# Optimization experiments

Measured on AMD Instinct MI355X. Metric: run time of the kernel, lower is better.

## Reference

```python
import jax, jax.numpy as jnp
import numpy as np

# PercentClosenessBoosting (not in provided source): standard form is
#   new_boost = boost_tensor + (1 - tensor / tensor.max()) * boost_percent
# i.e. units far from the max get boosted more.

def _fwd_math(x, boost_tensor, sparsity, boost_percent):
    B, E = x.shape
    # --- run_boosting ---
    new_boost = boost_tensor + (1.0 - x / jnp.max(x)) * boost_percent
    boosted = jnp.maximum(x, 0.0) + new_boost
    # inhibition tensor starts empty -> apply_sparse_self_affector is a no-op
    # --- run_k_winners_positive: top-k (max_active) per row of boosted, binarize ---
    order = jnp.argsort(-boosted, axis=1)          # descending sort indices
    rank = jnp.argsort(order, axis=1)              # rank of each element in its row
    max_active = jnp.ceil(sparsity[1] * E)
    saved = jnp.where((rank < max_active) & (boosted > 0), 1.0, 0.0)  # ctx.save_for_backward
    # --- choose_boosted_to_satisfy_minimum (note: GLOBAL sum vs per-row min, faithful) ---
    min_active = jnp.floor(sparsity[0] * E)
    active = jnp.sum(saved)
    to_activate = jnp.ceil(min_active - active)
    border = jnp.argsort(-new_boost, axis=1)
    brank = jnp.argsort(border, axis=1)
    need = active < min_active
    out = jnp.where(need & (brank < to_activate), 1.0, saved)
    # --- zero boost where active ---
    final_boost = jnp.where(out > 0, jnp.zeros_like(new_boost), new_boost)
    return out, final_boost, saved


def setup_inputs() -> dict:
    key = jax.random.key(0)
    k1, = jax.random.split(key, 1)
    B, E = 64, 131072
    x = jax.random.normal(k1, (B, E), dtype=jnp.float32)
    boost_tensor = jnp.zeros((B, E), dtype=jnp.float32)
    sparsity = jnp.array([0.002, 0.02], dtype=jnp.float32)
    boost_percent = jnp.float32(1e-8)
    return {"x": x, "boost_tensor": boost_tensor, "sparsity": sparsity, "boost_percent": boost_percent}


def reference(x, boost_tensor, sparsity, boost_percent):
    out, final_boost, _ = _fwd_math(x, boost_tensor, sparsity, boost_percent)
    return out, final_boost
```

## Files before the change

kernel.cpp:

```cpp
#include <hip/hip_runtime.h>

#define BR 64
#define EC 131072
#define CAP 8192
#define LCAP 1024
#define CHUNKS 16
#define CHUNK_V (EC / CHUNKS / 4)
#define NSCH 41
#define NS (NSCH * 64)
#define SSTRIDE 3197
#define BINS 4096

typedef float nf4 __attribute__((ext_vector_type(4)));

#define WS_GMAX 0
#define WS_ACTIVE 1
#define WS_TOACT 2
#define WS_UT 136
#define WS_CUT 200
#define WS_CCNT 264
#define WS_UT2 512
#define WS_CUT2 576
#define WS_BMAX 1024
#define CAND_U_OFF 4096
#define CAND_I_OFF (CAND_U_OFF + BR * CAP)

__device__ __forceinline__ unsigned map_f(float f) {
    unsigned b = __float_as_uint(f);
    return (b & 0x80000000u) ? ~b : (b | 0x80000000u);
}
__device__ __forceinline__ float unmap_f(unsigned u) {
    unsigned b = (u & 0x80000000u) ? (u & 0x7FFFFFFFu) : ~u;
    return __uint_as_float(b);
}

__device__ __forceinline__ void compute_vals(float x, float bt, float gmax, float bp,
                                             float* nb, float* bo) {
#pragma clang fp contract(off)
    float q = x / gmax;
    float t = 1.0f - q;
    float p = t * bp;
    float nbv = bt + p;
    *nb = nbv;
    *bo = fmaxf(x, 0.0f) + nbv;
}

__device__ __forceinline__ unsigned umax_(unsigned a, unsigned b) { return a > b ? a : b; }

__device__ __forceinline__ unsigned calc_K(const float* sp) {
    unsigned K = (unsigned)ceilf(sp[1] * (float)EC);
    if (K > EC) K = EC;
    if (K == 0) K = 1;
    return K;
}

__device__ unsigned lds_radix_select(const unsigned* su, unsigned n, unsigned K,
                                     unsigned* hist, unsigned* scan, unsigned* sb,
                                     int t, unsigned* krem) {
    unsigned pv = 0, Kp = K;
    for (int pass = 0; pass < 4; ++pass) {
        int shift = 24 - 8 * pass;
        hist[t] = 0;
        __syncthreads();
        for (unsigned i = t; i < n; i += 256) {
            unsigned u = su[i];
            bool match = (pass == 0) || ((u >> (shift + 8)) == (pv >> (shift + 8)));
            if (match) atomicAdd(&hist[(u >> shift) & 0xFFu], 1u);
        }
        __syncthreads();
        unsigned my = hist[t];
        scan[t] = my;
        __syncthreads();
        for (int off = 1; off < 256; off <<= 1) {
            unsigned v = (t + off < 256) ? scan[t + off] : 0u;
            __syncthreads();
            scan[t] += v;
            __syncthreads();
        }
        unsigned incl = scan[t], excl = incl - my;
        if (excl < Kp && incl >= Kp) {
            sb[0] = pv | ((unsigned)t << shift);
            sb[1] = Kp - excl;
        }
        __syncthreads();
        pv = sb[0];
        Kp = sb[1];
        __syncthreads();
    }
    *krem = Kp;
    return pv;
}

template<int USE_NB>
__device__ unsigned row_select_full(const float* xr, const float* br, float gmax,
                                    float bp, unsigned K, unsigned* hist,
                                    unsigned* aux, int t,
                                    unsigned* ut_out, unsigned* cut_out) {
    unsigned prefix = 0, Kp = K;
    for (int pass = 0; pass < 4; ++pass) {
        int shift = 24 - 8 * pass;
        hist[t] = 0;
        __syncthreads();
        for (int i = t; i < EC; i += 256) {
            float nb, bo;
            compute_vals(xr[i], br[i], gmax, bp, &nb, &bo);
            unsigned u = map_f(USE_NB ? nb : bo);
            bool match = (pass == 0) || ((u >> (shift + 8)) == (prefix >> (shift + 8)));
            if (match) atomicAdd(&hist[(u >> shift) & 0xFFu], 1u);
        }
        __syncthreads();
        if (t == 0) {
            unsigned cum = 0, bsel = 0, kr = Kp;
            for (int b = 255; b >= 0; --b) {
                unsigned h = hist[b];
                if (cum + h >= Kp) { bsel = (unsigned)b; kr = Kp - cum; break; }
                cum += h;
            }
            aux[0] = prefix | (bsel << shift);
            aux[1] = kr;
        }
        __syncthreads();
        prefix = aux[0];
        Kp = aux[1];
        __syncthreads();
    }
    unsigned u_t = prefix, ties = Kp;
    if (t == 0) { aux[6] = 0; aux[7] = 0xFFFFFFFFu; }
    __syncthreads();
    int wid = t >> 6, lane = t & 63;
    for (int base0 = 0; base0 < EC; base0 += 256) {
        int i = base0 + t;
        float nb, bo;
        compute_vals(xr[i], br[i], gmax, bp, &nb, &bo);
        bool eq = (map_f(USE_NB ? nb : bo) == u_t);
        unsigned long long bal = __ballot(eq);
        if (lane == 0) aux[2 + wid] = (unsigned)__popcll(bal);
        __syncthreads();
        unsigned run = aux[6];
        unsigned wpre = 0;
        for (int w = 0; w < wid; ++w) wpre += aux[2 + w];
        if (eq) {
            unsigned r = run + wpre + (unsigned)__popcll(bal & ((1ull << lane) - 1ull));
            if (r == ties - 1) aux[7] = (unsigned)i;
        }
        __syncthreads();
        if (t == 0) aux[6] = run + aux[2] + aux[3] + aux[4] + aux[5];
        __syncthreads();
        if (aux[6] >= ties) break;
    }
    if (t == 0) { *ut_out = u_t; *cut_out = aux[7]; }
    __syncthreads();
    return u_t;
}

__global__ __launch_bounds__(256) void kA(const float4* __restrict__ x4,
                                          unsigned* __restrict__ ws) {
    if (blockIdx.x == 0)
        for (int i = threadIdx.x; i < 1024; i += 256) ws[i] = 0u;
    unsigned m = 0;
    const int nvec = BR * EC / 4;
    int stride = gridDim.x * 256;
    for (int v = blockIdx.x * 256 + threadIdx.x; v < nvec; v += stride) {
        float4 xv = x4[v];
        m = umax_(m, map_f(xv.x)); m = umax_(m, map_f(xv.y));
        m = umax_(m, map_f(xv.z)); m = umax_(m, map_f(xv.w));
    }
    for (int off = 32; off; off >>= 1) m = umax_(m, __shfl_down(m, off, 64));
    __shared__ unsigned sm[4];
    if ((threadIdx.x & 63) == 0) sm[threadIdx.x >> 6] = m;
    __syncthreads();
    if (threadIdx.x == 0)
        ws[WS_BMAX + blockIdx.x] = umax_(umax_(sm[0], sm[1]), umax_(sm[2], sm[3]));
}

__global__ __launch_bounds__(256) void kB(const float* __restrict__ x,
                                          const float* __restrict__ bt,
                                          const float* __restrict__ sp,
                                          const float* __restrict__ bp_p,
                                          unsigned* __restrict__ ws) {
    __shared__ unsigned hist[BINS];
    __shared__ unsigned lu[LCAP], li[LCAP];
    __shared__ unsigned ssum[256], sabove[256];
    __shared__ unsigned sred[4];
    __shared__ unsigned stlo, slcnt, sgbase;
    int t = threadIdx.x;
    int row = blockIdx.x >> 4, chunk = blockIdx.x & (CHUNKS - 1);

    unsigned m = 0;
    for (int i = t; i < 1024; i += 256) m = umax_(m, ws[WS_BMAX + i]);
    for (int off = 32; off; off >>= 1) m = umax_(m, __shfl_down(m, off, 64));
    if ((t & 63) == 0) sred[t >> 6] = m;
    __syncthreads();
    unsigned gmu = umax_(umax_(sred[0], sred[1]), umax_(sred[2], sred[3]));
    if (blockIdx.x == 0 && t == 0) ws[WS_GMAX] = gmu;
    float gmax = unmap_f(gmu);
    float bp = *bp_p;

    for (int i = t; i < BINS; i += 256) hist[i] = 0;
    if (t == 0) slcnt = 0;
    __syncthreads();
    const float* xr = x + (size_t)row * EC;
    const float* br = bt + (size_t)row * EC;
    for (int s = t; s < NS; s += 256) {
        int idx = (s >> 6) * SSTRIDE + (s & 63);
        float nb, bo;
        compute_vals(xr[idx], br[idx], gmax, bp, &nb, &bo);
        atomicAdd(&hist[map_f(bo) >> 20], 1u);
    }
    __syncthreads();

    unsigned K = calc_K(sp);
    unsigned R = (unsigned)ceilf(1.75f * (float)NS * (float)K / (float)EC);
    if (R < 32) R = 32;
    if (R > NS) R = NS;
    unsigned hv[16];
    unsigned s = 0;
    #pragma unroll
    for (int j = 0; j < 16; ++j) { hv[j] = hist[t * 16 + j]; s += hv[j]; }
    ssum[t] = s;
    __syncthreads();
    if (t == 0) {
        unsigned acc = 0;
        for (int q = 255; q >= 0; --q) { sabove[q] = acc; acc += ssum[q]; }
    }
    __syncthreads();
    unsigned cum = sabove[t];
    for (int j = 15; j >= 0; --j) {
        unsigned h = hv[j];
        if (cum < R && cum + h >= R) stlo = ((unsigned)(t * 16 + j)) << 20;
        cum += h;
    }
    __syncthreads();
    unsigned tlo = stlo ? stlo - 1u : 0u;

    const float4* x4 = (const float4*)x;
    const float4* bt4 = (const float4*)bt;
    unsigned* cu = ws + CAND_U_OFF + (size_t)row * CAP;
    unsigned* ci = ws + CAND_I_OFF + (size_t)row * CAP;
    size_t base = (size_t)row * (EC / 4) + (size_t)chunk * CHUNK_V;
    int ebase = chunk * (EC / CHUNKS);
    for (int v = t; v < CHUNK_V; v += 256) {
        float4 xv = x4[base + v];
        float4 bv = bt4[base + v];
        float xs[4] = {xv.x, xv.y, xv.z, xv.w};
        float bs[4] = {bv.x, bv.y, bv.z, bv.w};
        #pragma unroll
        for (int j = 0; j < 4; ++j) {
            float nb, bo;
            compute_vals(xs[j], bs[j], gmax, bp, &nb, &bo);
            unsigned u = map_f(bo);
            if (u > tlo) {
                unsigned p = atomicAdd(&slcnt, 1u);
                if (p < LCAP) {
                    lu[p] = u; li[p] = (unsigned)(ebase + v * 4 + j);
                } else {
                    unsigned gp = atomicAdd(&ws[WS_CCNT + row], 1u);
                    if (gp < CAP) { cu[gp] = u; ci[gp] = (unsigned)(ebase + v * 4 + j); }
                }
            }
        }
    }
    __syncthreads();
    unsigned n = slcnt < LCAP ? slcnt : LCAP;
    if (t == 0) sgbase = atomicAdd(&ws[WS_CCNT + row], n);
    __syncthreads();
    unsigned gb = sgbase;
    for (unsigned i = t; i < n; i += 256) {
        unsigned gp = gb + i;
        if (gp < CAP) { cu[gp] = lu[i]; ci[gp] = li[i]; }
    }
}

__global__ __launch_bounds__(256) void kC(const float* __restrict__ x,
                                          const float* __restrict__ bt,
                                          const float* __restrict__ sp,
                                          const float* __restrict__ bp_p,
                                          unsigned* __restrict__ ws) {
    int row = blockIdx.x;
    int t = threadIdx.x;
    unsigned n = ws[WS_CCNT + row];
    unsigned K = calc_K(sp);
    __shared__ unsigned su[CAP];
    __shared__ unsigned hist[256], scan[256], sb[2];
    __shared__ unsigned marr[256];
    __shared__ unsigned mcnt;
    __shared__ unsigned aux[8];
    __shared__ unsigned scnt[4];
    unsigned row_active = 0;
    if (n >= K && n <= CAP) {
        const unsigned* cu = ws + CAND_U_OFF + (size_t)row * CAP;
        const unsigned* ci = ws + CAND_I_OFF + (size_t)row * CAP;
        for (unsigned i = t; i < n; i += 256) su[i] = cu[i];
        if (t == 0) mcnt = 0;
        __syncthreads();
        unsigned krem2;
        unsigned u_t = lds_radix_select(su, n, K, hist, scan, sb, t, &krem2);
        for (unsigned i = t; i < n; i += 256)
            if (su[i] == u_t) {
                unsigned p = atomicAdd(&mcnt, 1u);
                if (p < 256) marr[p] = ci[i];
            }
        __syncthreads();
        unsigned m = mcnt;
        if (m <= 256) {
            for (unsigned i = t; i < m; i += 256) {
                unsigned myidx = marr[i];
                unsigned r = 0;
                for (unsigned j = 0; j < m; ++j) r += (marr[j] < myidx) ? 1u : 0u;
                if (r == krem2 - 1) { ws[WS_UT + row] = u_t; ws[WS_CUT + row] = myidx; }
            }
        } else {
            for (unsigned i = t; i < n; i += 256) {
                if (su[i] == u_t) {
                    unsigned myidx = ci[i];
                    unsigned r = 0;
                    for (unsigned j = 0; j < n; ++j)
                        if (su[j] == u_t && ci[j] < myidx) ++r;
                    if (r == krem2 - 1) { ws[WS_UT + row] = u_t; ws[WS_CUT + row] = myidx; }
                }
            }
        }
        if (u_t > 0x80000000u) {
            row_active = K;
        } else {
            unsigned c = 0;
            for (unsigned i = t; i < n; i += 256) c += (su[i] > 0x80000000u) ? 1u : 0u;
            for (int off = 32; off; off >>= 1) c += __shfl_down(c, off, 64);
            if ((t & 63) == 0) scnt[t >> 6] = c;
            __syncthreads();
            row_active = scnt[0] + scnt[1] + scnt[2] + scnt[3];
        }
    } else {
        float gmax = unmap_f(ws[WS_GMAX]);
        float bp = *bp_p;
        const float* xr = x + (size_t)row * EC;
        const float* br = bt + (size_t)row * EC;
        unsigned u_t = row_select_full<0>(xr, br, gmax, bp, K, hist, aux, t,
                                          &ws[WS_UT + row], &ws[WS_CUT + row]);
        if (u_t > 0x80000000u) {
            row_active = K;
        } else {
            unsigned c = 0;
            for (int i = t; i < EC; i += 256) {
                float nb, bo;
                compute_vals(xr[i], br[i], gmax, bp, &nb, &bo);
                c += (map_f(bo) > 0x80000000u) ? 1u : 0u;
            }
            for (int off = 32; off; off >>= 1) c += __shfl_down(c, off, 64);
            if ((t & 63) == 0) scnt[t >> 6] = c;
            __syncthreads();
            row_active = scnt[0] + scnt[1] + scnt[2] + scnt[3];
        }
    }
    if (t == 0) atomicAdd(&ws[WS_ACTIVE], row_active);
}

__global__ __launch_bounds__(256) void kD(const float* __restrict__ x,
                                          const float* __restrict__ bt,
                                          const float* __restrict__ sp,
                                          const float* __restrict__ bp_p,
                                          unsigned* ws) {
    float min_active = floorf(sp[0] * (float)EC);
    float active = (float)ws[WS_ACTIVE];
    if (!(active < min_active)) return;
    unsigned K = (unsigned)ceilf(min_active - active);
    if (blockIdx.x == 0 && threadIdx.x == 0) ws[WS_TOACT] = K;
    if (K > EC) K = EC;
    int row = blockIdx.x;
    float gmax = unmap_f(ws[WS_GMAX]);
    float bp = *bp_p;
    __shared__ unsigned hist[256];
    __shared__ unsigned aux[8];
    row_select_full<1>(x + (size_t)row * EC, bt + (size_t)row * EC, gmax, bp, K,
                       hist, aux, threadIdx.x, &ws[WS_UT2 + row], &ws[WS_CUT2 + row]);
}

__global__ void kE(const float4* __restrict__ x4, const float4* __restrict__ bt4,
                   const float* __restrict__ bp_p, const unsigned* __restrict__ ws,
                   nf4* __restrict__ out4, nf4* __restrict__ fb4) {
    float gmax = unmap_f(ws[WS_GMAX]);
    float bp = *bp_p;
    unsigned toact = ws[WS_TOACT];
    const size_t nvec = (size_t)BR * EC / 4;
    size_t stride = (size_t)gridDim.x * blockDim.x;
    for (size_t v = (size_t)blockIdx.x * blockDim.x + threadIdx.x; v < nvec; v += stride) {
        size_t e0 = v << 2;
        int row = (int)(e0 >> 17);
        int col = (int)(e0 & (size_t)(EC - 1));
        unsigned u_t = ws[WS_UT + row];
        int cut = (int)ws[WS_CUT + row];
        float4 xv = x4[v], bv = bt4[v];
        float xarr[4] = {xv.x, xv.y, xv.z, xv.w};
        float barr[4] = {bv.x, bv.y, bv.z, bv.w};
        nf4 o, f;
        #pragma unroll
        for (int j = 0; j < 4; ++j) {
            float nb, bo;
            compute_vals(xarr[j], barr[j], gmax, bp, &nb, &bo);
            unsigned u = map_f(bo);
            bool sel = (u > u_t) || ((u == u_t) && ((col + j) <= cut));
            bool saved = sel && (u > 0x80000000u);
            o[j] = saved ? 1.0f : 0.0f;
            f[j] = saved ? 0.0f : nb;
        }
        if (toact) {
            unsigned ut2 = ws[WS_UT2 + row];
            int cut2 = (int)ws[WS_CUT2 + row];
            #pragma unroll
            for (int j = 0; j < 4; ++j) {
                float nb, bo;
                compute_vals(xarr[j], barr[j], gmax, bp, &nb, &bo);
                unsigned u2 = map_f(nb);
                if (u2 > ut2 || (u2 == ut2 && (col + j) <= cut2)) {
                    o[j] = 1.0f;
                    f[j] = 0.0f;
                }
            }
        }
        __builtin_nontemporal_store(o, &out4[v]);
        __builtin_nontemporal_store(f, &fb4[v]);
    }
}

extern "C" void kernel_launch(void* const* d_in, const int* in_sizes, int n_in,
                              void* d_out, int out_size, void* d_ws, size_t ws_size,
                              hipStream_t stream) {
    const float* x  = (const float*)d_in[0];
    const float* bt = (const float*)d_in[1];
    const float* sp = (const float*)d_in[2];
    const float* bp = (const float*)d_in[3];
    float* out = (float*)d_out;
    float* fb  = out + (size_t)BR * EC;
    unsigned* ws = (unsigned*)d_ws;

    kA<<<1024, 256, 0, stream>>>((const float4*)x, ws);
    kB<<<BR * CHUNKS, 256, 0, stream>>>(x, bt, sp, bp, ws);
    kC<<<BR, 256, 0, stream>>>(x, bt, sp, bp, ws);
    kD<<<BR, 256, 0, stream>>>(x, bt, sp, bp, ws);
    kE<<<2048, 256, 0, stream>>>((const float4*)x, (const float4*)bt, bp, ws,
                                 (nf4*)out, (nf4*)fb);
}
```

Baseline: 77.54 us.

## Count positives in candidate pass and fold min-active selection into kC

Each kB block now counts positive boosted values per row and accumulates them in the workspace, so the active count per row becomes min(K, positives) instead of being recounted in kC. With every kC block able to compute the global active sum itself, the separate kD launch is removed and its minimum-activation selection runs inside kC. This removes a kernel launch, a global atomic dependency and redundant counting loops. It adds a warp reduction and an atomic to kB, and it relies on the new counter being zeroed beforehand.

```diff
diff --git a/kernel.cpp b/kernel.cpp
--- a/kernel.cpp
+++ b/kernel.cpp
@@ -14,13 +14,13 @@
 typedef float nf4 __attribute__((ext_vector_type(4)));
 
 #define WS_GMAX 0
-#define WS_ACTIVE 1
 #define WS_TOACT 2
 #define WS_UT 136
 #define WS_CUT 200
 #define WS_CCNT 264
 #define WS_UT2 512
 #define WS_CUT2 576
+#define WS_NPOS 640
 #define WS_BMAX 1024
 #define CAND_U_OFF 4096
 #define CAND_I_OFF (CAND_U_OFF + BR * CAP)
@@ -46,6 +46,7 @@
 }
 
 __device__ __forceinline__ unsigned umax_(unsigned a, unsigned b) { return a > b ? a : b; }
+__device__ __forceinline__ unsigned umin_(unsigned a, unsigned b) { return a < b ? a : b; }
 
 __device__ __forceinline__ unsigned calc_K(const float* sp) {
     unsigned K = (unsigned)ceilf(sp[1] * (float)EC);
@@ -239,6 +240,7 @@
     unsigned* ci = ws + CAND_I_OFF + (size_t)row * CAP;
     size_t base = (size_t)row * (EC / 4) + (size_t)chunk * CHUNK_V;
     int ebase = chunk * (EC / CHUNKS);
+    unsigned posc = 0;
     for (int v = t; v < CHUNK_V; v += 256) {
         float4 xv = x4[base + v];
         float4 bv = bt4[base + v];
@@ -249,6 +251,7 @@
             float nb, bo;
             compute_vals(xs[j], bs[j], gmax, bp, &nb, &bo);
             unsigned u = map_f(bo);
+            posc += (u > 0x80000000u) ? 1u : 0u;
             if (u > tlo) {
                 unsigned p = atomicAdd(&slcnt, 1u);
                 if (p < LCAP) {
@@ -260,6 +263,10 @@
             }
         }
     }
+    for (int off = 32; off; off >>= 1) posc += __shfl_down(posc, off, 64);
+    if ((t & 63) == 0) sred[t >> 6] = posc;
+    __syncthreads();
+    if (t == 0) atomicAdd(&ws[WS_NPOS + row], sred[0] + sred[1] + sred[2] + sred[3]);
     __syncthreads();
     unsigned n = slcnt < LCAP ? slcnt : LCAP;
     if (t == 0) sgbase = atomicAdd(&ws[WS_CCNT + row], n);
@@ -280,13 +287,14 @@
     int t = threadIdx.x;
     unsigned n = ws[WS_CCNT + row];
     unsigned K = calc_K(sp);
+    float gmax = unmap_f(ws[WS_GMAX]);
+    float bp = *bp_p;
     __shared__ unsigned su[CAP];
     __shared__ unsigned hist[256], scan[256], sb[2];
     __shared__ unsigned marr[256];
     __shared__ unsigned mcnt;
     __shared__ unsigned aux[8];
-    __shared__ unsigned scnt[4];
-    unsigned row_active = 0;
+    __shared__ unsigned sact;
     if (n >= K && n <= CAP) {
         const unsigned* cu = ws + CAND_U_OFF + (size_t)row * CAP;
         const unsigned* ci = ws + CAND_I_OFF + (size_t)row * CAP;
@@ -320,59 +328,25 @@
                 }
             }
         }
-        if (u_t > 0x80000000u) {
-            row_active = K;
-        } else {
-            unsigned c = 0;
-            for (unsigned i = t; i < n; i += 256) c += (su[i] > 0x80000000u) ? 1u : 0u;
-            for (int off = 32; off; off >>= 1) c += __shfl_down(c, off, 64);
-            if ((t & 63) == 0) scnt[t >> 6] = c;
-            __syncthreads();
-            row_active = scnt[0] + scnt[1] + scnt[2] + scnt[3];
-        }
     } else {
-        float gmax = unmap_f(ws[WS_GMAX]);
-        float bp = *bp_p;
-        const float* xr = x + (size_t)row * EC;
-        const float* br = bt + (size_t)row * EC;
-        unsigned u_t = row_select_full<0>(xr, br, gmax, bp, K, hist, aux, t,
-                                          &ws[WS_UT + row], &ws[WS_CUT + row]);
-        if (u_t > 0x80000000u) {
-            row_active = K;
-        } else {
-            unsigned c = 0;
-            for (int i = t; i < EC; i += 256) {
-                float nb, bo;
-                compute_vals(xr[i], br[i], gmax, bp, &nb, &bo);
-                c += (map_f(bo) > 0x80000000u) ? 1u : 0u;
-            }
-            for (int off = 32; off; off >>= 1) c += __shfl_down(c, off, 64);
-            if ((t & 63) == 0) scnt[t >> 6] = c;
-            __syncthreads();
-            row_active = scnt[0] + scnt[1] + scnt[2] + scnt[3];
-        }
-    }
-    if (t == 0) atomicAdd(&ws[WS_ACTIVE], row_active);
-}
-
-__global__ __launch_bounds__(256) void kD(const float* __restrict__ x,
-                                          const float* __restrict__ bt,
-                                          const float* __restrict__ sp,
-                                          const float* __restrict__ bp_p,
-                                          unsigned* ws) {
+        row_select_full<0>(x + (size_t)row * EC, bt + (size_t)row * EC, gmax, bp, K,
+                           hist, aux, t, &ws[WS_UT + row], &ws[WS_CUT + row]);
+    }
+
+    unsigned act = 0;
+    if (t < 64) act = umin_(K, ws[WS_NPOS + t]);
+    for (int off = 32; off; off >>= 1) act += __shfl_down(act, off, 64);
+    if (t == 0) sact = act;
+    __syncthreads();
+    float active = (float)sact;
     float min_active = floorf(sp[0] * (float)EC);
-    float active = (float)ws[WS_ACTIVE];
-    if (!(active < min_active)) return;
-    unsigned K = (unsigned)ceilf(min_active - active);
-    if (blockIdx.x == 0 && threadIdx.x == 0) ws[WS_TOACT] = K;
-    if (K > EC) K = EC;
-    int row = blockIdx.x;
-    float gmax = unmap_f(ws[WS_GMAX]);
-    float bp = *bp_p;
-    __shared__ unsigned hist[256];
-    __shared__ unsigned aux[8];
-    row_select_full<1>(x + (size_t)row * EC, bt + (size_t)row * EC, gmax, bp, K,
-                       hist, aux, threadIdx.x, &ws[WS_UT2 + row], &ws[WS_CUT2 + row]);
+    if (active < min_active) {
+        unsigned K2 = (unsigned)ceilf(min_active - active);
+        if (row == 0 && t == 0) ws[WS_TOACT] = K2;
+        if (K2 > EC) K2 = EC;
+        row_select_full<1>(x + (size_t)row * EC, bt + (size_t)row * EC, gmax, bp, K2,
+                           hist, aux, t, &ws[WS_UT2 + row], &ws[WS_CUT2 + row]);
+    }
 }
 
 __global__ void kE(const float4* __restrict__ x4, const float4* __restrict__ bt4,
@@ -436,7 +410,6 @@
     kA<<<1024, 256, 0, stream>>>((const float4*)x, ws);
     kB<<<BR * CHUNKS, 256, 0, stream>>>(x, bt, sp, bp, ws);
     kC<<<BR, 256, 0, stream>>>(x, bt, sp, bp, ws);
-    kD<<<BR, 256, 0, stream>>>(x, bt, sp, bp, ws);
     kE<<<2048, 256, 0, stream>>>((const float4*)x, (const float4*)bt, bp, ws,
                                  (nf4*)out, (nf4*)fb);
 }
```

New measurement: 76.69 us. No clear change (-1.1%).
